# Performance work log

Hardware: AMD Instinct MI355X
Metric: run time of the kernel (lower is better)

The kernel has to match this reference:

```python
import jax, jax.numpy as jnp
import numpy as np

L, B, T, D, H, F, V = 4, 2, 1024, 1024, 16, 4096, 32000
DH = D // H
POWER = 4
EPS = 1e-6


def _anorm(x, gain):
    # y = g * x / (mean(|x|) + eps)  (L1 'diamond' norm)
    return gain * (x / (jnp.mean(jnp.abs(x), axis=-1, keepdims=True) + EPS))


def _rational_softmax(x):
    s = x / (jnp.abs(x) + 1.0)          # squash to (-1, 1)
    p = ((s + 1.0) * 0.5) ** POWER      # shift to (0,1), sharpen
    return p / (jnp.sum(p, axis=-1, keepdims=True) + EPS)


def setup_inputs() -> dict:
    key = jax.random.key(0)
    ks = jax.random.split(key, 12)
    w = 0.02  # weight scale for stability
    return {
        "idx": jax.random.randint(ks[0], (B, T), 0, V),
        "tok_emb": jax.random.normal(ks[1], (V, D), jnp.float32) * w,
        "pos_emb": jax.random.normal(ks[2], (T, D), jnp.float32) * w,
        "Wq": jax.random.normal(ks[3], (L, D, D), jnp.float32) * w,
        "bq": jnp.zeros((L, D), jnp.float32),
        "Wk": jax.random.normal(ks[4], (L, D, D), jnp.float32) * w,
        "bk": jnp.zeros((L, D), jnp.float32),
        "Wv": jax.random.normal(ks[5], (L, D, D), jnp.float32) * w,
        "bv": jnp.zeros((L, D), jnp.float32),
        "Wo": jax.random.normal(ks[6], (L, D, D), jnp.float32) * w,
        "bo": jnp.zeros((L, D), jnp.float32),
        "score_gain": jnp.full((L,), 4.0, jnp.float32),
        "norm1_gain": jnp.ones((L, D), jnp.float32),
        "norm2_gain": jnp.ones((L, D), jnp.float32),
        "W1": jax.random.normal(ks[7], (L, D, F), jnp.float32) * w,
        "b1": jnp.zeros((L, F), jnp.float32),
        "W2": jax.random.normal(ks[8], (L, F, D), jnp.float32) * w,
        "b2": jnp.zeros((L, D), jnp.float32),
        "final_gain": jnp.ones((D,), jnp.float32),
        "Wlm": jax.random.normal(ks[9], (D, V), jnp.float32) * w,
        "blm": jnp.zeros((V,), jnp.float32),
    }


def _forward(idx, tok_emb, pos_emb, Wq, bq, Wk, bk, Wv, bv, Wo, bo,
             score_gain, norm1_gain, norm2_gain, W1, b1, W2, b2,
             final_gain, Wlm, blm):
    Bx, Tx = idx.shape
    x = tok_emb[idx] + pos_emb[:Tx]                 # [B,T,D]
    mask = jnp.triu(jnp.ones((Tx, Tx), bool), 1)    # causal mask (True = masked)
    for l in range(L):
        # --- algebraic attention ---
        h = _anorm(x, norm1_gain[l])
        q = (h @ Wq[l] + bq[l]).reshape(Bx, Tx, H, DH).transpose(0, 2, 1, 3)
        k = (h @ Wk[l] + bk[l]).reshape(Bx, Tx, H, DH).transpose(0, 2, 1, 3)
        v = (h @ Wv[l] + bv[l]).reshape(Bx, Tx, H, DH).transpose(0, 2, 1, 3)
        scores = jnp.einsum('bhqd,bhkd->bhqk', q, k)
        scores = scores - jnp.mean(scores, axis=-1, keepdims=True)
        mad = jnp.mean(jnp.abs(scores), axis=-1, keepdims=True) + EPS
        scores = (scores / mad) * score_gain[l]
        scores = jnp.where(mask, -1000.0, scores)
        attn = _rational_softmax(scores)
        o = jnp.einsum('bhqk,bhkd->bhqd', attn, v)
        o = o.transpose(0, 2, 1, 3).reshape(Bx, Tx, D)
        x = x + (o @ Wo[l] + bo[l])
        # --- FFN with algebraic ReLU ---
        h = _anorm(x, norm2_gain[l])
        h = jnp.maximum(h @ W1[l] + b1[l], 0.0)
        x = x + (h @ W2[l] + b2[l])
    x = _anorm(x, final_gain)
    return x @ Wlm + blm                            # [B,T,V] logits


def reference(idx, tok_emb, pos_emb, Wq, bq, Wk, bk, Wv, bv, Wo, bo,
              score_gain, norm1_gain, norm2_gain, W1, b1, W2, b2,
              final_gain, Wlm, blm):
    return _forward(idx, tok_emb, pos_emb, Wq, bq, Wk, bk, Wv, bv, Wo, bo,
                    score_gain, norm1_gain, norm2_gain, W1, b1, W2, b2,
                    final_gain, Wlm, blm)
```

## Files before the change

kernel.cpp:

```cpp
#include <hip/hip_runtime.h>

typedef unsigned short u16;
typedef __bf16 bf16x8 __attribute__((ext_vector_type(8)));
typedef float f32x4 __attribute__((ext_vector_type(4)));
typedef unsigned int u32;

#define EPSF 1e-6f

__device__ __forceinline__ u16 f2bf(float f) {
  union { float f; unsigned u; } un; un.f = f;
  unsigned r = un.u + 0x7FFFu + ((un.u >> 16) & 1u);
  return (u16)(r >> 16);
}

__device__ __forceinline__ float block_sum(float v) {
  #pragma unroll
  for (int off = 32; off > 0; off >>= 1) v += __shfl_xor(v, off, 64);
  __shared__ float ws[4];
  const int w = threadIdx.x >> 6;
  __syncthreads();
  if ((threadIdx.x & 63) == 0) ws[w] = v;
  __syncthreads();
  return ws[0] + ws[1] + ws[2] + ws[3];
}

__device__ __forceinline__ void lds_cp16(const void* g, void* l) {
  __builtin_amdgcn_global_load_lds(
      (__attribute__((address_space(1))) void*)g,
      (__attribute__((address_space(3))) void*)l, 16, 0, 0);
}

__global__ __launch_bounds__(256) void embed_norm(
    const int* __restrict__ idx, const float* __restrict__ tok,
    const float* __restrict__ pos, const float* __restrict__ gain,
    float* __restrict__ x, u16* __restrict__ h) {
  const int row = blockIdx.x;
  const int tpos = row & 1023;
  const int token = idx[row];
  const int d = threadIdx.x * 4;
  const float4 a = *(const float4*)(tok + (long)token * 1024 + d);
  const float4 b = *(const float4*)(pos + (long)tpos * 1024 + d);
  float4 o; o.x = a.x + b.x; o.y = a.y + b.y; o.z = a.z + b.z; o.w = a.w + b.w;
  *(float4*)(x + (long)row * 1024 + d) = o;
  float s = fabsf(o.x) + fabsf(o.y) + fabsf(o.z) + fabsf(o.w);
  s = block_sum(s);
  const float scale = 1.0f / (s * (1.0f / 1024.0f) + EPSF);
  const float4 g = *(const float4*)(gain + d);
  ushort4 ov;
  ov.x = f2bf(o.x * g.x * scale);
  ov.y = f2bf(o.y * g.y * scale);
  ov.z = f2bf(o.z * g.z * scale);
  ov.w = f2bf(o.w * g.w * scale);
  *(ushort4*)(h + (long)row * 1024 + d) = ov;
}

__global__ __launch_bounds__(256) void anorm_kernel(
    const float* __restrict__ x, const float* __restrict__ gain,
    u16* __restrict__ h) {
  const int row = blockIdx.x;
  const int tid = threadIdx.x;
  const float4 v = *(const float4*)(x + (long)row * 1024 + tid * 4);
  float s = fabsf(v.x) + fabsf(v.y) + fabsf(v.z) + fabsf(v.w);
  s = block_sum(s);
  const float scale = 1.0f / (s * (1.0f / 1024.0f) + EPSF);
  const float4 g = *(const float4*)(gain + tid * 4);
  ushort4 o;
  o.x = f2bf(v.x * g.x * scale);
  o.y = f2bf(v.y * g.y * scale);
  o.z = f2bf(v.z * g.z * scale);
  o.w = f2bf(v.w * g.w * scale);
  *(ushort4*)(h + (long)row * 1024 + tid * 4) = o;
}

__global__ __launch_bounds__(512, 4) void attn_v4(
    const u16* __restrict__ qkv, const u16* __restrict__ v_t,
    u16* __restrict__ obuf, const float* __restrict__ score_gain, int l) {
  __shared__ float red1[2][4][16], red2[2][4][16], red3[2][4][16];
  __shared__ float Ured[2][4][16][68];
  __shared__ u16 Pl[8][640];
  const int qt = blockIdx.x, h = blockIdx.y, b = blockIdx.z;
  const int tid = threadIdx.x, w = tid >> 6, l64 = tid & 63;
  const int lq = l64 & 15, kgrp = l64 >> 4;
  const int wq = w >> 2, tq = w & 3;
  const int qglob = qt * 32 + wq * 16 + lq;
  const int qmax  = qt * 32 + wq * 16 + 15;
  const int tbase = tq * 256;
  const u16* Qg = qkv + (size_t)b * (1024 * 3072) + h * 64;
  const u16* Kg = Qg + 1024;
  const u16* Vt = v_t + (size_t)(b * 16 + h) * (64 * 1024);
  char* Pw = (char*)&Pl[w][0];

  bf16x8 qB0, qB1;
  {
    const u16* qp = Qg + (size_t)qglob * 3072 + (kgrp << 3);
    qB0 = *(const bf16x8*)qp;
    qB1 = *(const bf16x8*)(qp + 32);
  }

  f32x4 s[16];
  {
    const u16* Kl = Kg + (size_t)(tbase + lq) * 3072 + (kgrp << 3);
    #pragma unroll
    for (int tile = 0; tile < 16; tile++) {
      const u16* kp = Kl + (size_t)tile * (16 * 3072);
      const bf16x8 k0 = *(const bf16x8*)kp;
      const bf16x8 k1 = *(const bf16x8*)(kp + 32);
      f32x4 d = {0.f, 0.f, 0.f, 0.f};
      d = __builtin_amdgcn_mfma_f32_16x16x32_bf16(k0, qB0, d, 0, 0, 0);
      d = __builtin_amdgcn_mfma_f32_16x16x32_bf16(k1, qB1, d, 0, 0, 0);
      s[tile] = d;
    }
  }

  float ssum = 0.f;
  #pragma unroll
  for (int tile = 0; tile < 16; tile++)
    ssum += (s[tile][0] + s[tile][1]) + (s[tile][2] + s[tile][3]);
  ssum += __shfl_xor(ssum, 16, 64);
  ssum += __shfl_xor(ssum, 32, 64);
  if (l64 < 16) red1[wq][tq][l64] = ssum;
  __syncthreads();
  const float mean = (red1[wq][0][lq] + red1[wq][1][lq] +
                      red1[wq][2][lq] + red1[wq][3][lq]) * (1.0f / 1024.0f);

  float asum = 0.f;
  #pragma unroll
  for (int tile = 0; tile < 16; tile++)
    asum += fabsf(s[tile][0] - mean) + fabsf(s[tile][1] - mean) +
            fabsf(s[tile][2] - mean) + fabsf(s[tile][3] - mean);
  asum += __shfl_xor(asum, 16, 64);
  asum += __shfl_xor(asum, 32, 64);
  if (l64 < 16) red2[wq][tq][l64] = asum;
  __syncthreads();
  const float mad = (red2[wq][0][lq] + red2[wq][1][lq] +
                     red2[wq][2][lq] + red2[wq][3][lq]) * (1.0f / 1024.0f) + EPSF;
  const float gs = score_gain[l] / mad;

  float psum = 0.f;
  #pragma unroll
  for (int tile = 0; tile < 16; tile++) {
    #pragma unroll
    for (int j = 0; j < 4; j++) {
      const int t = tbase + tile * 16 + (kgrp << 2) + j;
      float sv = (s[tile][j] - mean) * gs;
      if (t > qglob) sv = -1000.0f;
      const float rr = sv / (fabsf(sv) + 1.0f);
      const float a1 = (rr + 1.0f) * 0.5f;
      const float a2 = a1 * a1;
      s[tile][j] = a2 * a2;
      psum += s[tile][j];
    }
  }

  f32x4 U[4] = {};
  #pragma unroll
  for (int c = 0; c < 8; c++) {
    const int t0 = tbase + c * 32;
    if (t0 <= qmax) {
      #pragma unroll
      for (int half = 0; half < 2; half++) {
        #pragma unroll
        for (int pr = 0; pr < 2; pr++) {
          const u32 pk = (u32)f2bf(s[2 * c + half][pr * 2]) |
                         ((u32)f2bf(s[2 * c + half][pr * 2 + 1]) << 16);
          *(u32*)(Pw + lq * 80 + half * 32 + (kgrp << 3) + (pr << 2)) = pk;
        }
      }
      asm volatile("s_waitcnt lgkmcnt(0)" ::: "memory");
      __builtin_amdgcn_sched_barrier(0);
      const bf16x8 pB = *(const bf16x8*)(Pw + lq * 80 + (kgrp << 4));
      #pragma unroll
      for (int dt = 0; dt < 4; dt++) {
        const bf16x8 vA = *(const bf16x8*)(Vt + (size_t)((dt << 4) + lq) * 1024 +
                                           t0 + (kgrp << 3));
        U[dt] = __builtin_amdgcn_mfma_f32_16x16x32_bf16(vA, pB, U[dt], 0, 0, 0);
      }
    }
  }

  psum += __shfl_xor(psum, 16, 64);
  psum += __shfl_xor(psum, 32, 64);
  if (l64 < 16) red3[wq][tq][l64] = psum;
  #pragma unroll
  for (int dt = 0; dt < 4; dt++)
    *(float4*)&Ured[wq][tq][lq][(dt << 4) + (kgrp << 2)] = *(const float4*)&U[dt];
  __syncthreads();

  {
    const int qq = tid >> 4, dhseg = (tid & 15) << 2;
    const int fwq = qq >> 4, flq = qq & 15;
    const float fps = red3[fwq][0][flq] + red3[fwq][1][flq] +
                      red3[fwq][2][flq] + red3[fwq][3][flq];
    const float oinv = 1.0f / (fps + EPSF);
    float4 u0 = *(const float4*)&Ured[fwq][0][flq][dhseg];
    const float4 u1 = *(const float4*)&Ured[fwq][1][flq][dhseg];
    const float4 u2 = *(const float4*)&Ured[fwq][2][flq][dhseg];
    const float4 u3 = *(const float4*)&Ured[fwq][3][flq][dhseg];
    u0.x = (u0.x + u1.x + u2.x + u3.x) * oinv;
    u0.y = (u0.y + u1.y + u2.y + u3.y) * oinv;
    u0.z = (u0.z + u1.z + u2.z + u3.z) * oinv;
    u0.w = (u0.w + u1.w + u2.w + u3.w) * oinv;
    ushort4 o;
    o.x = f2bf(u0.x); o.y = f2bf(u0.y); o.z = f2bf(u0.z); o.w = f2bf(u0.w);
    u16* dst = obuf + ((size_t)((b << 10) + qt * 32 + qq) << 10) + (h << 6) + dhseg;
    *(ushort4*)dst = o;
  }
}

__global__ void wconv_all(
    const float* __restrict__ Wq, const float* __restrict__ Wk,
    const float* __restrict__ Wv, const float* __restrict__ Wo,
    const float* __restrict__ W1, const float* __restrict__ W2,
    const float* __restrict__ Wlm,
    u16* __restrict__ wqkv_t, u16* __restrict__ wo_t,
    u16* __restrict__ w1_t, u16* __restrict__ w2_t, u16* __restrict__ wlm_t) {
  __shared__ float tile[64][65];
  const int bid = blockIdx.x;
  const float* src; u16* dst; int R, C, c0, r0;
  if (bid < 4096) {
    const int l = bid >> 10, m = (bid >> 8) & 3, t = bid & 255;
    if (m == 0)      src = Wq + (size_t)l * 1048576;
    else if (m == 1) src = Wk + (size_t)l * 1048576;
    else if (m == 2) src = Wv + (size_t)l * 1048576;
    else             src = Wo + (size_t)l * 1048576;
    dst = (m < 3) ? wqkv_t + ((size_t)l * 3072 + m * 1024) * 1024
                  : wo_t + (size_t)l * 1048576;
    R = 1024; C = 1024; c0 = (t & 15) << 6; r0 = (t >> 4) << 6;
  } else if (bid < 8192) {
    const int i = bid - 4096, l = i >> 10, t = i & 1023;
    src = W1 + (size_t)l * 4194304; dst = w1_t + (size_t)l * 4194304;
    R = 1024; C = 4096; c0 = (t & 63) << 6; r0 = (t >> 6) << 6;
  } else if (bid < 12288) {
    const int i = bid - 8192, l = i >> 10, t = i & 1023;
    src = W2 + (size_t)l * 4194304; dst = w2_t + (size_t)l * 4194304;
    R = 4096; C = 1024; c0 = (t & 15) << 6; r0 = (t >> 4) << 6;
  } else {
    const int i = bid - 12288;
    src = Wlm; dst = wlm_t;
    R = 1024; C = 32000; c0 = (i % 500) << 6; r0 = (i / 500) << 6;
  }
  const int tx = threadIdx.x, ty = threadIdx.y;
  #pragma unroll
  for (int i = 0; i < 16; i++)
    tile[i * 4 + ty][tx] = src[(long)(r0 + i * 4 + ty) * C + c0 + tx];
  __syncthreads();
  #pragma unroll
  for (int i = 0; i < 16; i++)
    dst[(long)(c0 + i * 4 + ty) * R + r0 + tx] = f2bf(tile[tx][i * 4 + ty]);
}

__global__ __launch_bounds__(256) void build_vt(
    const u16* __restrict__ qkv, u16* __restrict__ v_t) {
  __shared__ u16 tile[32][33];
  const int z = blockIdx.z, b = z >> 4, h = z & 15;
  const u16* src = qkv + (long)b * 1024 * 3072 + 2048 + h * 64;
  u16* dst = v_t + (long)z * 64 * 1024;
  const int t0 = blockIdx.x * 32, d0 = blockIdx.y * 32;
  const int tx = threadIdx.x, ty = threadIdx.y;
  #pragma unroll
  for (int i = 0; i < 4; i++)
    tile[ty + 8 * i][tx] = src[(long)(t0 + ty + 8 * i) * 3072 + d0 + tx];
  __syncthreads();
  #pragma unroll
  for (int i = 0; i < 4; i++)
    dst[(long)(d0 + ty + 8 * i) * 1024 + t0 + tx] = tile[tx][ty + 8 * i];
}

__global__ __launch_bounds__(256) void bias_concat(
    const float* __restrict__ bq, const float* __restrict__ bk,
    const float* __restrict__ bv, float* __restrict__ out) {
  const int i = blockIdx.x * 256 + threadIdx.x;
  const int l = i / 3072, j = i % 3072;
  float v;
  if (j < 1024)      v = bq[l * 1024 + j];
  else if (j < 2048) v = bk[l * 1024 + j - 1024];
  else               v = bv[l * 1024 + j - 2048];
  out[i] = v;
}

__global__ __launch_bounds__(256) void ffn2_reduce_norm(
    const float* __restrict__ part, const float* __restrict__ b2,
    float* __restrict__ x, const float* __restrict__ gain,
    u16* __restrict__ h) {
  const int row = blockIdx.x, c = threadIdx.x * 4;
  const float4 p0 = *(const float4*)(part + (size_t)row * 1024 + c);
  const float4 p1 = *(const float4*)(part + (size_t)(row + 2048) * 1024 + c);
  const float4 bb = *(const float4*)(b2 + c);
  float4 xv = *(float4*)(x + (size_t)row * 1024 + c);
  xv.x += p0.x + p1.x + bb.x;
  xv.y += p0.y + p1.y + bb.y;
  xv.z += p0.z + p1.z + bb.z;
  xv.w += p0.w + p1.w + bb.w;
  *(float4*)(x + (size_t)row * 1024 + c) = xv;
  float s = fabsf(xv.x) + fabsf(xv.y) + fabsf(xv.z) + fabsf(xv.w);
  s = block_sum(s);
  const float scale = 1.0f / (s * (1.0f / 1024.0f) + EPSF);
  const float4 g = *(const float4*)(gain + c);
  ushort4 o;
  o.x = f2bf(xv.x * g.x * scale);
  o.y = f2bf(xv.y * g.y * scale);
  o.z = f2bf(xv.z * g.z * scale);
  o.w = f2bf(xv.w * g.w * scale);
  *(ushort4*)(h + (size_t)row * 1024 + c) = o;
}

template <bool OUT_BF16, bool BIAS, bool RELU, bool RESID>
__global__ __launch_bounds__(512) void gemm256_kernel(
    const u16* __restrict__ A, long lda,
    const u16* __restrict__ Bt, long ldb,
    void* __restrict__ Cv, long ldc,
    const float* __restrict__ bias, const float* __restrict__ resid,
    int M, int N, int K, int nTM) {
  __shared__ u16 lds[65536];
  const int nwg = gridDim.x;
  const int qx = nwg >> 3, rx = nwg & 7;
  const int xcd = blockIdx.x & 7, seq = blockIdx.x >> 3;
  const int wg = (xcd < rx ? xcd * (qx + 1) : rx * (qx + 1) + (xcd - rx) * qx) + seq;
  const int tm = wg % nTM, tn = wg / nTM;
  const int rowA0 = tm * 256, rowB0 = tn * 256;

  const int t = threadIdx.x, w = t >> 6, l = t & 63;
  const int lrow = l & 15, kgrp = l >> 4;
  const int wr = w >> 2, wc = w & 3;

  const int srow = t >> 2;
  const int scol = ((t & 3) ^ ((t >> 3) & 3)) * 8;
  const u16* Asrc = A + (long)(rowA0 + srow) * lda + scol;
  const u16* Bsrc = Bt + (long)(rowB0 + srow) * ldb + scol;
  char* ldsB = (char*)lds;
  const int wbase = w * 1024;

  const int fswz = (kgrp ^ ((lrow >> 1) & 3)) * 8;
  const int aoff = (wr * 128 + lrow) * 32 + fswz;
  const int boff = 8192 + (wc * 64 + lrow) * 32 + fswz;

  f32x4 acc[8][4] = {};
  const int NT = K >> 5;

  #pragma unroll
  for (int pt = 0; pt < 3; pt++) {
    const int k0 = pt << 5;
    const int bb = pt * 32768;
    lds_cp16(Asrc + k0,                    ldsB + bb + wbase);
    lds_cp16(Asrc + (long)128 * lda + k0,  ldsB + bb + 8192 + wbase);
    lds_cp16(Bsrc + k0,                    ldsB + bb + 16384 + wbase);
    lds_cp16(Bsrc + (long)128 * ldb + k0,  ldsB + bb + 24576 + wbase);
  }

  for (int tt = 0; tt < NT; tt++) {
    const int rem = NT - 1 - tt;
    if (rem >= 2)      asm volatile("s_waitcnt vmcnt(8)" ::: "memory");
    else if (rem == 1) asm volatile("s_waitcnt vmcnt(4)" ::: "memory");
    else               asm volatile("s_waitcnt vmcnt(0)" ::: "memory");
    __builtin_amdgcn_sched_barrier(0);
    __builtin_amdgcn_s_barrier();

    const u16* buf = lds + (tt & 3) * 16384;
    const int stage = tt + 3 < NT;
    const int k0n = (tt + 3) << 5;
    const int bbn = ((tt + 3) & 3) * 32768;

    bf16x8 aF[4], bF[4], aS[4];
    #pragma unroll
    for (int m = 0; m < 4; m++) aF[m] = *(const bf16x8*)(buf + aoff + m * 512);
    #pragma unroll
    for (int n = 0; n < 4; n++) bF[n] = *(const bf16x8*)(buf + boff + n * 512);
    __builtin_amdgcn_sched_barrier(0);
    #pragma unroll
    for (int m = 0; m < 4; m++) aS[m] = *(const bf16x8*)(buf + aoff + (m + 4) * 512);
    if (stage) {
      lds_cp16(Asrc + k0n,                   ldsB + bbn + wbase);
      lds_cp16(Asrc + (long)128 * lda + k0n, ldsB + bbn + 8192 + wbase);
      lds_cp16(Bsrc + k0n,                   ldsB + bbn + 16384 + wbase);
      lds_cp16(Bsrc + (long)128 * ldb + k0n, ldsB + bbn + 24576 + wbase);
    }
    asm volatile("s_waitcnt lgkmcnt(4)" ::: "memory");
    __builtin_amdgcn_sched_barrier(0);
    __builtin_amdgcn_s_setprio(1);
    #pragma unroll
    for (int m = 0; m < 4; m++)
      #pragma unroll
      for (int n = 0; n < 4; n++)
        acc[m][n] = __builtin_amdgcn_mfma_f32_16x16x32_bf16(aF[m], bF[n], acc[m][n], 0, 0, 0);
    __builtin_amdgcn_s_setprio(0);
    asm volatile("s_waitcnt lgkmcnt(0)" ::: "memory");
    __builtin_amdgcn_sched_barrier(0);
    __builtin_amdgcn_s_setprio(1);
    #pragma unroll
    for (int m = 0; m < 4; m++)
      #pragma unroll
      for (int n = 0; n < 4; n++)
        acc[m + 4][n] = __builtin_amdgcn_mfma_f32_16x16x32_bf16(aS[m], bF[n], acc[m + 4][n], 0, 0, 0);
    __builtin_amdgcn_s_setprio(0);
  }

  float bvv[4];
  #pragma unroll
  for (int n = 0; n < 4; n++)
    bvv[n] = BIAS ? bias[rowB0 + wc * 64 + n * 16 + lrow] : 0.0f;
  #pragma unroll
  for (int m = 0; m < 8; m++) {
    const int row = rowA0 + wr * 128 + m * 16 + kgrp * 4;
    #pragma unroll
    for (int n = 0; n < 4; n++) {
      const int col = rowB0 + wc * 64 + n * 16 + lrow;
      #pragma unroll
      for (int j = 0; j < 4; j++) {
        float v = acc[m][n][j] + bvv[n];
        if (RELU) v = fmaxf(v, 0.0f);
        const long off = (long)(row + j) * ldc + col;
        if (RESID) v += resid[off];
        if (OUT_BF16) ((u16*)Cv)[off] = f2bf(v);
        else          ((float*)Cv)[off] = v;
      }
    }
  }
}

template <bool OUT_BF16, bool BIAS, bool RELU, bool RESID>
__global__ __launch_bounds__(256) void gemm128p(
    const u16* __restrict__ A, long lda, long sA,
    const u16* __restrict__ Bt, long ldb, long sB,
    void* __restrict__ Cv, long ldc, long sC,
    const float* __restrict__ bias, const float* __restrict__ resid,
    int M, int N, int K, int nTM) {
  __shared__ u16 lds[32768];
  const int nwg = gridDim.x;
  const int qx = nwg >> 3, rx = nwg & 7;
  const int xcd = blockIdx.x & 7, seq = blockIdx.x >> 3;
  const int wg = (xcd < rx ? xcd * (qx + 1) : rx * (qx + 1) + (xcd - rx) * qx) + seq;
  const int tm = wg % nTM, tn = wg / nTM;
  const int batch = blockIdx.y;
  A  += (long)batch * sA;
  Bt += (long)batch * sB;
  const int rowA0 = tm * 128, rowB0 = tn * 128;
  const int t = threadIdx.x, w = t >> 6, l = t & 63;
  const int lrow = l & 15, kgrp = l >> 4;
  const int wr = (w >> 1) << 6, wc = (w & 1) << 6;

  const int srow = t >> 2;
  const int scol = ((t & 3) ^ ((t >> 3) & 3)) * 8;
  const u16* Asrc = A + (long)(rowA0 + srow) * lda + scol;
  const u16* Bsrc = Bt + (long)(rowB0 + srow) * ldb + scol;
  char* ldsB = (char*)lds;
  const int wbase = w * 1024;

  const int swz8 = (kgrp ^ ((lrow >> 1) & 3)) * 8;
  const int aoff = (wr + lrow) * 32 + swz8;
  const int boff = 4096 + (wc + lrow) * 32 + swz8;

  f32x4 acc[4][4] = {};
  const int NT = K >> 5;

  #pragma unroll
  for (int pt = 0; pt < 3; pt++) {
    const int k0 = pt << 5;
    const int bb = pt * 16384;
    lds_cp16(Asrc + k0,                   ldsB + bb + wbase);
    lds_cp16(Asrc + (long)64 * lda + k0,  ldsB + bb + 4096 + wbase);
    lds_cp16(Bsrc + k0,                   ldsB + bb + 8192 + wbase);
    lds_cp16(Bsrc + (long)64 * ldb + k0,  ldsB + bb + 12288 + wbase);
  }

  for (int tt = 0; tt < NT; tt++) {
    const int rem = NT - 1 - tt;
    if (rem >= 2)      asm volatile("s_waitcnt vmcnt(8)" ::: "memory");
    else if (rem == 1) asm volatile("s_waitcnt vmcnt(4)" ::: "memory");
    else               asm volatile("s_waitcnt vmcnt(0)" ::: "memory");
    __builtin_amdgcn_sched_barrier(0);
    __builtin_amdgcn_s_barrier();

    const u16* buf = lds + (tt & 3) * 8192;
    const int stage = tt + 3 < NT;
    const int k0n = (tt + 3) << 5;
    const int bbn = ((tt + 3) & 3) * 16384;

    bf16x8 aF[4], bF[4];
    #pragma unroll
    for (int m = 0; m < 4; m++) aF[m] = *(const bf16x8*)(buf + aoff + m * 512);
    #pragma unroll
    for (int n = 0; n < 4; n++) bF[n] = *(const bf16x8*)(buf + boff + n * 512);
    if (stage) {
      lds_cp16(Asrc + k0n,                  ldsB + bbn + wbase);
      lds_cp16(Asrc + (long)64 * lda + k0n, ldsB + bbn + 4096 + wbase);
      lds_cp16(Bsrc + k0n,                  ldsB + bbn + 8192 + wbase);
      lds_cp16(Bsrc + (long)64 * ldb + k0n, ldsB + bbn + 12288 + wbase);
    }
    asm volatile("s_waitcnt lgkmcnt(0)" ::: "memory");
    __builtin_amdgcn_sched_barrier(0);
    __builtin_amdgcn_s_setprio(1);
    #pragma unroll
    for (int m = 0; m < 4; m++)
      #pragma unroll
      for (int n = 0; n < 4; n++)
        acc[m][n] = __builtin_amdgcn_mfma_f32_16x16x32_bf16(aF[m], bF[n], acc[m][n], 0, 0, 0);
    __builtin_amdgcn_s_setprio(0);
  }

  const long coff = (long)batch * sC;
  #pragma unroll
  for (int m = 0; m < 4; m++) {
    #pragma unroll
    for (int n = 0; n < 4; n++) {
      const int col = rowB0 + wc + n * 16 + lrow;
      #pragma unroll
      for (int j = 0; j < 4; j++) {
        const int row = rowA0 + wr + m * 16 + (kgrp << 2) + j;
        float v = acc[m][n][j];
        if (BIAS) v += bias[col];
        if (RELU) v = fmaxf(v, 0.0f);
        const long off = coff + (long)row * ldc + col;
        if (RESID) v += resid[off];
        if (OUT_BF16) ((u16*)Cv)[off] = f2bf(v);
        else          ((float*)Cv)[off] = v;
      }
    }
  }
}

extern "C" void kernel_launch(void* const* d_in, const int* in_sizes, int n_in,
                              void* d_out, int out_size, void* d_ws, size_t ws_size,
                              hipStream_t stream) {
  constexpr int Lc = 4, Tc = 1024, Dc = 1024, Hc = 16, Fc = 4096, DHc = 64;
  const int M = 2 * Tc;

  const int*   idxp       = (const int*)  d_in[0];
  const float* tok_emb    = (const float*)d_in[1];
  const float* pos_emb    = (const float*)d_in[2];
  const float* Wq         = (const float*)d_in[3];
  const float* bq         = (const float*)d_in[4];
  const float* Wk         = (const float*)d_in[5];
  const float* bk         = (const float*)d_in[6];
  const float* Wv         = (const float*)d_in[7];
  const float* bv         = (const float*)d_in[8];
  const float* Wo         = (const float*)d_in[9];
  const float* bo         = (const float*)d_in[10];
  const float* score_gain = (const float*)d_in[11];
  const float* norm1_gain = (const float*)d_in[12];
  const float* norm2_gain = (const float*)d_in[13];
  const float* W1         = (const float*)d_in[14];
  const float* b1         = (const float*)d_in[15];
  const float* W2         = (const float*)d_in[16];
  const float* b2         = (const float*)d_in[17];
  const float* final_gain = (const float*)d_in[18];
  const float* Wlm        = (const float*)d_in[19];
  const float* blm        = (const float*)d_in[20];

  char* p = (char*)d_ws;
  auto alloc = [&](size_t n) { char* r = p; p += (n + 255) & ~(size_t)255; return r; };
  u16*  wqkv_t = (u16*) alloc((size_t)Lc * 3072 * 1024 * 2);
  u16*  wo_t   = (u16*) alloc((size_t)Lc * 1024 * 1024 * 2);
  u16*  w1_t   = (u16*) alloc((size_t)Lc * 4096 * 1024 * 2);
  u16*  w2_t   = (u16*) alloc((size_t)Lc * 1024 * 4096 * 2);
  u16*  wlm_t  = (u16*) alloc((size_t)32000 * 1024 * 2);
  float* bqkv  = (float*)alloc((size_t)Lc * 3072 * 4);
  float* x     = (float*)alloc((size_t)M * 1024 * 4);
  u16*  hbuf   = (u16*) alloc((size_t)M * 1024 * 2);
  u16*  qkv    = (u16*) alloc((size_t)M * 3072 * 2);
  u16*  v_t    = (u16*) alloc((size_t)2 * Hc * DHc * Tc * 2);
  u16*  obuf   = (u16*) alloc((size_t)M * 1024 * 2);
  u16*  ffh    = (u16*) alloc((size_t)M * 4096 * 2);
  float* fpart = (float*)alloc((size_t)2 * M * 1024 * 4);

  wconv_all<<<20288, dim3(64, 4), 0, stream>>>(Wq, Wk, Wv, Wo, W1, W2, Wlm,
                                               wqkv_t, wo_t, w1_t, w2_t, wlm_t);
  bias_concat<<<48, 256, 0, stream>>>(bq, bk, bv, bqkv);
  embed_norm<<<M, 256, 0, stream>>>(idxp, tok_emb, pos_emb, norm1_gain, x, hbuf);

  for (int l = 0; l < Lc; l++) {
    gemm128p<true, true, false, false><<<dim3(16 * 24, 1), 256, 0, stream>>>(
        hbuf, 1024, 0, wqkv_t + (size_t)l * 3072 * 1024, 1024, 0,
        qkv, 3072, 0, bqkv + (size_t)l * 3072, nullptr, M, 3072, 1024, 16);
    build_vt<<<dim3(32, 2, 32), dim3(32, 8), 0, stream>>>(qkv, v_t);

    attn_v4<<<dim3(32, 16, 2), 512, 0, stream>>>(qkv, v_t, obuf, score_gain, l);

    gemm128p<false, true, false, true><<<dim3(16 * 8, 1), 256, 0, stream>>>(
        obuf, 1024, 0, wo_t + (size_t)l * 1024 * 1024, 1024, 0,
        x, 1024, 0, bo + (size_t)l * 1024, x, M, 1024, 1024, 16);
    anorm_kernel<<<M, 256, 0, stream>>>(x, norm2_gain + (size_t)l * Dc, hbuf);
    gemm256_kernel<true, true, true, false><<<dim3(128), 512, 0, stream>>>(
        hbuf, 1024, w1_t + (size_t)l * Fc * Dc, 1024,
        ffh, 4096, b1 + (size_t)l * Fc, nullptr, M, 4096, 1024, 8);
    gemm128p<false, false, false, false><<<dim3(128, 2), 256, 0, stream>>>(
        ffh, 4096, 2048, w2_t + (size_t)l * Dc * Fc, 4096, 2048,
        fpart, 1024, (long)M * 1024, nullptr, nullptr, M, 1024, 2048, 16);
    const float* gnext = (l < Lc - 1) ? (norm1_gain + (size_t)(l + 1) * Dc) : final_gain;
    ffn2_reduce_norm<<<M, 256, 0, stream>>>(fpart, b2 + (size_t)l * Dc, x, gnext, hbuf);
  }

  gemm256_kernel<false, true, false, false><<<dim3(1000), 512, 0, stream>>>(
      hbuf, 1024, wlm_t, 1024,
      d_out, 32000, blm, nullptr, M, 32000, 1024, 8);
}
```

Baseline: 1.013 ms.

## Fuse V transpose into QKV GEMM epilogue and use 128-tile GEMM everywhere

The QKV GEMM epilogue now writes the V columns straight into the transposed v_t layout through LDS, which removes the separate build_vt kernel. The 256x256 GEMM kernel is removed, and the FFN1 and LM-head GEMMs now run on the 128-tile kernel with more workgroups. The FFN2 split-K goes from 2 to 4 partitions, with a larger partial buffer and a wider reduction. Together these trade tile reuse for occupancy and better wave balance, at the cost of more partial-sum traffic.

```diff
diff --git a/kernel.cpp b/kernel.cpp
--- a/kernel.cpp
+++ b/kernel.cpp
@@ -249,23 +249,6 @@
     dst[(long)(c0 + i * 4 + ty) * R + r0 + tx] = f2bf(tile[tx][i * 4 + ty]);
 }
 
-__global__ __launch_bounds__(256) void build_vt(
-    const u16* __restrict__ qkv, u16* __restrict__ v_t) {
-  __shared__ u16 tile[32][33];
-  const int z = blockIdx.z, b = z >> 4, h = z & 15;
-  const u16* src = qkv + (long)b * 1024 * 3072 + 2048 + h * 64;
-  u16* dst = v_t + (long)z * 64 * 1024;
-  const int t0 = blockIdx.x * 32, d0 = blockIdx.y * 32;
-  const int tx = threadIdx.x, ty = threadIdx.y;
-  #pragma unroll
-  for (int i = 0; i < 4; i++)
-    tile[ty + 8 * i][tx] = src[(long)(t0 + ty + 8 * i) * 3072 + d0 + tx];
-  __syncthreads();
-  #pragma unroll
-  for (int i = 0; i < 4; i++)
-    dst[(long)(d0 + ty + 8 * i) * 1024 + t0 + tx] = tile[tx][ty + 8 * i];
-}
-
 __global__ __launch_bounds__(256) void bias_concat(
     const float* __restrict__ bq, const float* __restrict__ bk,
     const float* __restrict__ bv, float* __restrict__ out) {
@@ -285,12 +268,14 @@
   const int row = blockIdx.x, c = threadIdx.x * 4;
   const float4 p0 = *(const float4*)(part + (size_t)row * 1024 + c);
   const float4 p1 = *(const float4*)(part + (size_t)(row + 2048) * 1024 + c);
+  const float4 p2 = *(const float4*)(part + (size_t)(row + 4096) * 1024 + c);
+  const float4 p3 = *(const float4*)(part + (size_t)(row + 6144) * 1024 + c);
   const float4 bb = *(const float4*)(b2 + c);
   float4 xv = *(float4*)(x + (size_t)row * 1024 + c);
-  xv.x += p0.x + p1.x + bb.x;
-  xv.y += p0.y + p1.y + bb.y;
-  xv.z += p0.z + p1.z + bb.z;
-  xv.w += p0.w + p1.w + bb.w;
+  xv.x += (p0.x + p1.x) + (p2.x + p3.x) + bb.x;
+  xv.y += (p0.y + p1.y) + (p2.y + p3.y) + bb.y;
+  xv.z += (p0.z + p1.z) + (p2.z + p3.z) + bb.z;
+  xv.w += (p0.w + p1.w) + (p2.w + p3.w) + bb.w;
   *(float4*)(x + (size_t)row * 1024 + c) = xv;
   float s = fabsf(xv.x) + fabsf(xv.y) + fabsf(xv.z) + fabsf(xv.w);
   s = block_sum(s);
@@ -304,125 +289,13 @@
   *(ushort4*)(h + (size_t)row * 1024 + c) = o;
 }
 
-template <bool OUT_BF16, bool BIAS, bool RELU, bool RESID>
-__global__ __launch_bounds__(512) void gemm256_kernel(
-    const u16* __restrict__ A, long lda,
-    const u16* __restrict__ Bt, long ldb,
-    void* __restrict__ Cv, long ldc,
-    const float* __restrict__ bias, const float* __restrict__ resid,
-    int M, int N, int K, int nTM) {
-  __shared__ u16 lds[65536];
-  const int nwg = gridDim.x;
-  const int qx = nwg >> 3, rx = nwg & 7;
-  const int xcd = blockIdx.x & 7, seq = blockIdx.x >> 3;
-  const int wg = (xcd < rx ? xcd * (qx + 1) : rx * (qx + 1) + (xcd - rx) * qx) + seq;
-  const int tm = wg % nTM, tn = wg / nTM;
-  const int rowA0 = tm * 256, rowB0 = tn * 256;
-
-  const int t = threadIdx.x, w = t >> 6, l = t & 63;
-  const int lrow = l & 15, kgrp = l >> 4;
-  const int wr = w >> 2, wc = w & 3;
-
-  const int srow = t >> 2;
-  const int scol = ((t & 3) ^ ((t >> 3) & 3)) * 8;
-  const u16* Asrc = A + (long)(rowA0 + srow) * lda + scol;
-  const u16* Bsrc = Bt + (long)(rowB0 + srow) * ldb + scol;
-  char* ldsB = (char*)lds;
-  const int wbase = w * 1024;
-
-  const int fswz = (kgrp ^ ((lrow >> 1) & 3)) * 8;
-  const int aoff = (wr * 128 + lrow) * 32 + fswz;
-  const int boff = 8192 + (wc * 64 + lrow) * 32 + fswz;
-
-  f32x4 acc[8][4] = {};
-  const int NT = K >> 5;
-
-  #pragma unroll
-  for (int pt = 0; pt < 3; pt++) {
-    const int k0 = pt << 5;
-    const int bb = pt * 32768;
-    lds_cp16(Asrc + k0,                    ldsB + bb + wbase);
-    lds_cp16(Asrc + (long)128 * lda + k0,  ldsB + bb + 8192 + wbase);
-    lds_cp16(Bsrc + k0,                    ldsB + bb + 16384 + wbase);
-    lds_cp16(Bsrc + (long)128 * ldb + k0,  ldsB + bb + 24576 + wbase);
-  }
-
-  for (int tt = 0; tt < NT; tt++) {
-    const int rem = NT - 1 - tt;
-    if (rem >= 2)      asm volatile("s_waitcnt vmcnt(8)" ::: "memory");
-    else if (rem == 1) asm volatile("s_waitcnt vmcnt(4)" ::: "memory");
-    else               asm volatile("s_waitcnt vmcnt(0)" ::: "memory");
-    __builtin_amdgcn_sched_barrier(0);
-    __builtin_amdgcn_s_barrier();
-
-    const u16* buf = lds + (tt & 3) * 16384;
-    const int stage = tt + 3 < NT;
-    const int k0n = (tt + 3) << 5;
-    const int bbn = ((tt + 3) & 3) * 32768;
-
-    bf16x8 aF[4], bF[4], aS[4];
-    #pragma unroll
-    for (int m = 0; m < 4; m++) aF[m] = *(const bf16x8*)(buf + aoff + m * 512);
-    #pragma unroll
-    for (int n = 0; n < 4; n++) bF[n] = *(const bf16x8*)(buf + boff + n * 512);
-    __builtin_amdgcn_sched_barrier(0);
-    #pragma unroll
-    for (int m = 0; m < 4; m++) aS[m] = *(const bf16x8*)(buf + aoff + (m + 4) * 512);
-    if (stage) {
-      lds_cp16(Asrc + k0n,                   ldsB + bbn + wbase);
-      lds_cp16(Asrc + (long)128 * lda + k0n, ldsB + bbn + 8192 + wbase);
-      lds_cp16(Bsrc + k0n,                   ldsB + bbn + 16384 + wbase);
-      lds_cp16(Bsrc + (long)128 * ldb + k0n, ldsB + bbn + 24576 + wbase);
-    }
-    asm volatile("s_waitcnt lgkmcnt(4)" ::: "memory");
-    __builtin_amdgcn_sched_barrier(0);
-    __builtin_amdgcn_s_setprio(1);
-    #pragma unroll
-    for (int m = 0; m < 4; m++)
-      #pragma unroll
-      for (int n = 0; n < 4; n++)
-        acc[m][n] = __builtin_amdgcn_mfma_f32_16x16x32_bf16(aF[m], bF[n], acc[m][n], 0, 0, 0);
-    __builtin_amdgcn_s_setprio(0);
-    asm volatile("s_waitcnt lgkmcnt(0)" ::: "memory");
-    __builtin_amdgcn_sched_barrier(0);
-    __builtin_amdgcn_s_setprio(1);
-    #pragma unroll
-    for (int m = 0; m < 4; m++)
-      #pragma unroll
-      for (int n = 0; n < 4; n++)
-        acc[m + 4][n] = __builtin_amdgcn_mfma_f32_16x16x32_bf16(aS[m], bF[n], acc[m + 4][n], 0, 0, 0);
-    __builtin_amdgcn_s_setprio(0);
-  }
-
-  float bvv[4];
-  #pragma unroll
-  for (int n = 0; n < 4; n++)
-    bvv[n] = BIAS ? bias[rowB0 + wc * 64 + n * 16 + lrow] : 0.0f;
-  #pragma unroll
-  for (int m = 0; m < 8; m++) {
-    const int row = rowA0 + wr * 128 + m * 16 + kgrp * 4;
-    #pragma unroll
-    for (int n = 0; n < 4; n++) {
-      const int col = rowB0 + wc * 64 + n * 16 + lrow;
-      #pragma unroll
-      for (int j = 0; j < 4; j++) {
-        float v = acc[m][n][j] + bvv[n];
-        if (RELU) v = fmaxf(v, 0.0f);
-        const long off = (long)(row + j) * ldc + col;
-        if (RESID) v += resid[off];
-        if (OUT_BF16) ((u16*)Cv)[off] = f2bf(v);
-        else          ((float*)Cv)[off] = v;
-      }
-    }
-  }
-}
-
-template <bool OUT_BF16, bool BIAS, bool RELU, bool RESID>
+template <bool OUT_BF16, bool BIAS, bool RELU, bool RESID, bool VTOUT>
 __global__ __launch_bounds__(256) void gemm128p(
     const u16* __restrict__ A, long lda, long sA,
     const u16* __restrict__ Bt, long ldb, long sB,
     void* __restrict__ Cv, long ldc, long sC,
     const float* __restrict__ bias, const float* __restrict__ resid,
+    u16* __restrict__ vtout,
     int M, int N, int K, int nTM) {
   __shared__ u16 lds[32768];
   const int nwg = gridDim.x;
@@ -497,22 +370,54 @@
     __builtin_amdgcn_s_setprio(0);
   }
 
-  const long coff = (long)batch * sC;
-  #pragma unroll
-  for (int m = 0; m < 4; m++) {
-    #pragma unroll
-    for (int n = 0; n < 4; n++) {
-      const int col = rowB0 + wc + n * 16 + lrow;
-      #pragma unroll
-      for (int j = 0; j < 4; j++) {
-        const int row = rowA0 + wr + m * 16 + (kgrp << 2) + j;
-        float v = acc[m][n][j];
-        if (BIAS) v += bias[col];
-        if (RELU) v = fmaxf(v, 0.0f);
-        const long off = coff + (long)row * ldc + col;
-        if (RESID) v += resid[off];
-        if (OUT_BF16) ((u16*)Cv)[off] = f2bf(v);
-        else          ((float*)Cv)[off] = v;
+  if (VTOUT && rowB0 >= 2048) {
+    __syncthreads();
+    #pragma unroll
+    for (int m = 0; m < 4; m++) {
+      #pragma unroll
+      for (int n = 0; n < 4; n++) {
+        const int c = wc + n * 16 + lrow;
+        const int r = wr + m * 16 + (kgrp << 2);
+        ushort4 pk;
+        float v0 = acc[m][n][0], v1 = acc[m][n][1], v2 = acc[m][n][2], v3 = acc[m][n][3];
+        if (BIAS) {
+          const float bv = bias[rowB0 + c];
+          v0 += bv; v1 += bv; v2 += bv; v3 += bv;
+        }
+        pk.x = f2bf(v0); pk.y = f2bf(v1); pk.z = f2bf(v2); pk.w = f2bf(v3);
+        *(ushort4*)&lds[c * 136 + r] = pk;
+      }
+    }
+    __syncthreads();
+    {
+      const int c = t >> 1, half = t & 1;
+      const int dh = c & 63;
+      const int h = ((rowB0 - 2048) >> 6) + (c >> 6);
+      const int bb2 = rowA0 >> 10, t0 = rowA0 & 1023;
+      u16* dst = vtout + (((size_t)(bb2 * 16 + h)) << 16) + ((size_t)dh << 10) +
+                 t0 + half * 64;
+      #pragma unroll
+      for (int k = 0; k < 8; k++)
+        *(bf16x8*)(dst + k * 8) = *(const bf16x8*)&lds[c * 136 + half * 64 + k * 8];
+    }
+  } else {
+    const long coff = (long)batch * sC;
+    #pragma unroll
+    for (int m = 0; m < 4; m++) {
+      #pragma unroll
+      for (int n = 0; n < 4; n++) {
+        const int col = rowB0 + wc + n * 16 + lrow;
+        #pragma unroll
+        for (int j = 0; j < 4; j++) {
+          const int row = rowA0 + wr + m * 16 + (kgrp << 2) + j;
+          float v = acc[m][n][j];
+          if (BIAS) v += bias[col];
+          if (RELU) v = fmaxf(v, 0.0f);
+          const long off = coff + (long)row * ldc + col;
+          if (RESID) v += resid[off];
+          if (OUT_BF16) ((u16*)Cv)[off] = f2bf(v);
+          else          ((float*)Cv)[off] = v;
+        }
       }
     }
   }
@@ -560,7 +465,7 @@
   u16*  v_t    = (u16*) alloc((size_t)2 * Hc * DHc * Tc * 2);
   u16*  obuf   = (u16*) alloc((size_t)M * 1024 * 2);
   u16*  ffh    = (u16*) alloc((size_t)M * 4096 * 2);
-  float* fpart = (float*)alloc((size_t)2 * M * 1024 * 4);
+  float* fpart = (float*)alloc((size_t)4 * M * 1024 * 4);
 
   wconv_all<<<20288, dim3(64, 4), 0, stream>>>(Wq, Wk, Wv, Wo, W1, W2, Wlm,
                                                wqkv_t, wo_t, w1_t, w2_t, wlm_t);
@@ -568,28 +473,27 @@
   embed_norm<<<M, 256, 0, stream>>>(idxp, tok_emb, pos_emb, norm1_gain, x, hbuf);
 
   for (int l = 0; l < Lc; l++) {
-    gemm128p<true, true, false, false><<<dim3(16 * 24, 1), 256, 0, stream>>>(
+    gemm128p<true, true, false, false, true><<<dim3(16 * 24, 1), 256, 0, stream>>>(
         hbuf, 1024, 0, wqkv_t + (size_t)l * 3072 * 1024, 1024, 0,
-        qkv, 3072, 0, bqkv + (size_t)l * 3072, nullptr, M, 3072, 1024, 16);
-    build_vt<<<dim3(32, 2, 32), dim3(32, 8), 0, stream>>>(qkv, v_t);
+        qkv, 3072, 0, bqkv + (size_t)l * 3072, nullptr, v_t, M, 3072, 1024, 16);
 
     attn_v4<<<dim3(32, 16, 2), 512, 0, stream>>>(qkv, v_t, obuf, score_gain, l);
 
-    gemm128p<false, true, false, true><<<dim3(16 * 8, 1), 256, 0, stream>>>(
+    gemm128p<false, true, false, true, false><<<dim3(16 * 8, 1), 256, 0, stream>>>(
         obuf, 1024, 0, wo_t + (size_t)l * 1024 * 1024, 1024, 0,
-        x, 1024, 0, bo + (size_t)l * 1024, x, M, 1024, 1024, 16);
+        x, 1024, 0, bo + (size_t)l * 1024, x, nullptr, M, 1024, 1024, 16);
     anorm_kernel<<<M, 256, 0, stream>>>(x, norm2_gain + (size_t)l * Dc, hbuf);
-    gemm256_kernel<true, true, true, false><<<dim3(128), 512, 0, stream>>>(
-        hbuf, 1024, w1_t + (size_t)l * Fc * Dc, 1024,
-        ffh, 4096, b1 + (size_t)l * Fc, nullptr, M, 4096, 1024, 8);
-    gemm128p<false, false, false, false><<<dim3(128, 2), 256, 0, stream>>>(
-        ffh, 4096, 2048, w2_t + (size_t)l * Dc * Fc, 4096, 2048,
-        fpart, 1024, (long)M * 1024, nullptr, nullptr, M, 1024, 2048, 16);
+    gemm128p<true, true, true, false, false><<<dim3(16 * 32, 1), 256, 0, stream>>>(
+        hbuf, 1024, 0, w1_t + (size_t)l * Fc * Dc, 1024, 0,
+        ffh, 4096, 0, b1 + (size_t)l * Fc, nullptr, nullptr, M, 4096, 1024, 16);
+    gemm128p<false, false, false, false, false><<<dim3(128, 4), 256, 0, stream>>>(
+        ffh, 4096, 1024, w2_t + (size_t)l * Dc * Fc, 4096, 1024,
+        fpart, 1024, (long)M * 1024, nullptr, nullptr, nullptr, M, 1024, 1024, 16);
     const float* gnext = (l < Lc - 1) ? (norm1_gain + (size_t)(l + 1) * Dc) : final_gain;
     ffn2_reduce_norm<<<M, 256, 0, stream>>>(fpart, b2 + (size_t)l * Dc, x, gnext, hbuf);
   }
 
-  gemm256_kernel<false, true, false, false><<<dim3(1000), 512, 0, stream>>>(
-      hbuf, 1024, wlm_t, 1024,
-      d_out, 32000, blm, nullptr, M, 32000, 1024, 8);
-}
+  gemm128p<false, true, false, false, false><<<dim3(16 * 250, 1), 256, 0, stream>>>(
+      hbuf, 1024, 0, wlm_t, 1024, 0,
+      d_out, 32000, 0, blm, nullptr, nullptr, M, 32000, 1024, 16);
+}
```

Measured after the change: 1.022 ms. Within noise of the previous version (+0.8%).

## Fuse V-transpose into QKV GEMM, retile FFN GEMMs, vectorize weight conversion

Applied to the files above, without the earlier changes.

The QKV GEMM epilogue now writes V tiles transposed through LDS straight into v_t, so the separate build_vt kernel is dropped. FFN1 moves from the 256-tile kernel to the 128-tile kernel with more workgroups. FFN2 uses a 4-way split-K whose partials are reduced in the norm kernel, which doubles the partial-sum buffer traffic. The weight conversion uses float4 loads and ushort4 stores, and the 256 GEMM main loop staggers its A/B LDS loads to cut register pressure, at the cost of a full lgkmcnt wait.

```diff
diff --git a/kernel.cpp b/kernel.cpp
--- a/kernel.cpp
+++ b/kernel.cpp
@@ -240,30 +240,24 @@
     R = 1024; C = 32000; c0 = (i % 500) << 6; r0 = (i / 500) << 6;
   }
   const int tx = threadIdx.x, ty = threadIdx.y;
-  #pragma unroll
-  for (int i = 0; i < 16; i++)
-    tile[i * 4 + ty][tx] = src[(long)(r0 + i * 4 + ty) * C + c0 + tx];
+  const int cg = (tx & 15) << 2;
+  const int rg = tx >> 4;
+  #pragma unroll
+  for (int i = 0; i < 4; i++) {
+    const int row = i * 16 + ty * 4 + rg;
+    const float4 v = *(const float4*)&src[(long)(r0 + row) * C + c0 + cg];
+    tile[row][cg] = v.x; tile[row][cg + 1] = v.y;
+    tile[row][cg + 2] = v.z; tile[row][cg + 3] = v.w;
+  }
   __syncthreads();
   #pragma unroll
-  for (int i = 0; i < 16; i++)
-    dst[(long)(c0 + i * 4 + ty) * R + r0 + tx] = f2bf(tile[tx][i * 4 + ty]);
-}
-
-__global__ __launch_bounds__(256) void build_vt(
-    const u16* __restrict__ qkv, u16* __restrict__ v_t) {
-  __shared__ u16 tile[32][33];
-  const int z = blockIdx.z, b = z >> 4, h = z & 15;
-  const u16* src = qkv + (long)b * 1024 * 3072 + 2048 + h * 64;
-  u16* dst = v_t + (long)z * 64 * 1024;
-  const int t0 = blockIdx.x * 32, d0 = blockIdx.y * 32;
-  const int tx = threadIdx.x, ty = threadIdx.y;
-  #pragma unroll
-  for (int i = 0; i < 4; i++)
-    tile[ty + 8 * i][tx] = src[(long)(t0 + ty + 8 * i) * 3072 + d0 + tx];
-  __syncthreads();
-  #pragma unroll
-  for (int i = 0; i < 4; i++)
-    dst[(long)(d0 + ty + 8 * i) * 1024 + t0 + tx] = tile[tx][ty + 8 * i];
+  for (int i = 0; i < 4; i++) {
+    const int c = i * 16 + ty * 4 + rg;
+    ushort4 o;
+    o.x = f2bf(tile[cg][c]);     o.y = f2bf(tile[cg + 1][c]);
+    o.z = f2bf(tile[cg + 2][c]); o.w = f2bf(tile[cg + 3][c]);
+    *(ushort4*)&dst[(long)(c0 + c) * R + r0 + cg] = o;
+  }
 }
 
 __global__ __launch_bounds__(256) void bias_concat(
@@ -285,12 +279,14 @@
   const int row = blockIdx.x, c = threadIdx.x * 4;
   const float4 p0 = *(const float4*)(part + (size_t)row * 1024 + c);
   const float4 p1 = *(const float4*)(part + (size_t)(row + 2048) * 1024 + c);
+  const float4 p2 = *(const float4*)(part + (size_t)(row + 4096) * 1024 + c);
+  const float4 p3 = *(const float4*)(part + (size_t)(row + 6144) * 1024 + c);
   const float4 bb = *(const float4*)(b2 + c);
   float4 xv = *(float4*)(x + (size_t)row * 1024 + c);
-  xv.x += p0.x + p1.x + bb.x;
-  xv.y += p0.y + p1.y + bb.y;
-  xv.z += p0.z + p1.z + bb.z;
-  xv.w += p0.w + p1.w + bb.w;
+  xv.x += (p0.x + p1.x) + (p2.x + p3.x) + bb.x;
+  xv.y += (p0.y + p1.y) + (p2.y + p3.y) + bb.y;
+  xv.z += (p0.z + p1.z) + (p2.z + p3.z) + bb.z;
+  xv.w += (p0.w + p1.w) + (p2.w + p3.w) + bb.w;
   *(float4*)(x + (size_t)row * 1024 + c) = xv;
   float s = fabsf(xv.x) + fabsf(xv.y) + fabsf(xv.z) + fabsf(xv.w);
   s = block_sum(s);
@@ -360,21 +356,16 @@
     const int k0n = (tt + 3) << 5;
     const int bbn = ((tt + 3) & 3) * 32768;
 
-    bf16x8 aF[4], bF[4], aS[4];
+    bf16x8 aF[4], bF[4];
     #pragma unroll
     for (int m = 0; m < 4; m++) aF[m] = *(const bf16x8*)(buf + aoff + m * 512);
     #pragma unroll
     for (int n = 0; n < 4; n++) bF[n] = *(const bf16x8*)(buf + boff + n * 512);
-    __builtin_amdgcn_sched_barrier(0);
-    #pragma unroll
-    for (int m = 0; m < 4; m++) aS[m] = *(const bf16x8*)(buf + aoff + (m + 4) * 512);
     if (stage) {
       lds_cp16(Asrc + k0n,                   ldsB + bbn + wbase);
       lds_cp16(Asrc + (long)128 * lda + k0n, ldsB + bbn + 8192 + wbase);
-      lds_cp16(Bsrc + k0n,                   ldsB + bbn + 16384 + wbase);
-      lds_cp16(Bsrc + (long)128 * ldb + k0n, ldsB + bbn + 24576 + wbase);
-    }
-    asm volatile("s_waitcnt lgkmcnt(4)" ::: "memory");
+    }
+    asm volatile("s_waitcnt lgkmcnt(0)" ::: "memory");
     __builtin_amdgcn_sched_barrier(0);
     __builtin_amdgcn_s_setprio(1);
     #pragma unroll
@@ -383,6 +374,13 @@
       for (int n = 0; n < 4; n++)
         acc[m][n] = __builtin_amdgcn_mfma_f32_16x16x32_bf16(aF[m], bF[n], acc[m][n], 0, 0, 0);
     __builtin_amdgcn_s_setprio(0);
+
+    #pragma unroll
+    for (int m = 0; m < 4; m++) aF[m] = *(const bf16x8*)(buf + aoff + (m + 4) * 512);
+    if (stage) {
+      lds_cp16(Bsrc + k0n,                   ldsB + bbn + 16384 + wbase);
+      lds_cp16(Bsrc + (long)128 * ldb + k0n, ldsB + bbn + 24576 + wbase);
+    }
     asm volatile("s_waitcnt lgkmcnt(0)" ::: "memory");
     __builtin_amdgcn_sched_barrier(0);
     __builtin_amdgcn_s_setprio(1);
@@ -390,7 +388,7 @@
     for (int m = 0; m < 4; m++)
       #pragma unroll
       for (int n = 0; n < 4; n++)
-        acc[m + 4][n] = __builtin_amdgcn_mfma_f32_16x16x32_bf16(aS[m], bF[n], acc[m + 4][n], 0, 0, 0);
+        acc[m + 4][n] = __builtin_amdgcn_mfma_f32_16x16x32_bf16(aF[m], bF[n], acc[m + 4][n], 0, 0, 0);
     __builtin_amdgcn_s_setprio(0);
   }
 
@@ -417,12 +415,13 @@
   }
 }
 
-template <bool OUT_BF16, bool BIAS, bool RELU, bool RESID>
+template <bool OUT_BF16, bool BIAS, bool RELU, bool RESID, bool VTOUT>
 __global__ __launch_bounds__(256) void gemm128p(
     const u16* __restrict__ A, long lda, long sA,
     const u16* __restrict__ Bt, long ldb, long sB,
     void* __restrict__ Cv, long ldc, long sC,
     const float* __restrict__ bias, const float* __restrict__ resid,
+    u16* __restrict__ vtout,
     int M, int N, int K, int nTM) {
   __shared__ u16 lds[32768];
   const int nwg = gridDim.x;
@@ -497,22 +496,54 @@
     __builtin_amdgcn_s_setprio(0);
   }
 
-  const long coff = (long)batch * sC;
-  #pragma unroll
-  for (int m = 0; m < 4; m++) {
-    #pragma unroll
-    for (int n = 0; n < 4; n++) {
-      const int col = rowB0 + wc + n * 16 + lrow;
-      #pragma unroll
-      for (int j = 0; j < 4; j++) {
-        const int row = rowA0 + wr + m * 16 + (kgrp << 2) + j;
-        float v = acc[m][n][j];
-        if (BIAS) v += bias[col];
-        if (RELU) v = fmaxf(v, 0.0f);
-        const long off = coff + (long)row * ldc + col;
-        if (RESID) v += resid[off];
-        if (OUT_BF16) ((u16*)Cv)[off] = f2bf(v);
-        else          ((float*)Cv)[off] = v;
+  if (VTOUT && rowB0 >= 2048) {
+    __syncthreads();
+    #pragma unroll
+    for (int m = 0; m < 4; m++) {
+      #pragma unroll
+      for (int n = 0; n < 4; n++) {
+        const int c = wc + n * 16 + lrow;
+        const int r = wr + m * 16 + (kgrp << 2);
+        ushort4 pk;
+        float v0 = acc[m][n][0], v1 = acc[m][n][1], v2 = acc[m][n][2], v3 = acc[m][n][3];
+        if (BIAS) {
+          const float bv = bias[rowB0 + c];
+          v0 += bv; v1 += bv; v2 += bv; v3 += bv;
+        }
+        pk.x = f2bf(v0); pk.y = f2bf(v1); pk.z = f2bf(v2); pk.w = f2bf(v3);
+        *(ushort4*)&lds[c * 136 + r] = pk;
+      }
+    }
+    __syncthreads();
+    {
+      const int c = t >> 1, half = t & 1;
+      const int dh = c & 63;
+      const int h = ((rowB0 - 2048) >> 6) + (c >> 6);
+      const int bb2 = rowA0 >> 10, t0 = rowA0 & 1023;
+      u16* dst = vtout + (((size_t)(bb2 * 16 + h)) << 16) + ((size_t)dh << 10) +
+                 t0 + half * 64;
+      #pragma unroll
+      for (int k = 0; k < 8; k++)
+        *(bf16x8*)(dst + k * 8) = *(const bf16x8*)&lds[c * 136 + half * 64 + k * 8];
+    }
+  } else {
+    const long coff = (long)batch * sC;
+    #pragma unroll
+    for (int m = 0; m < 4; m++) {
+      #pragma unroll
+      for (int n = 0; n < 4; n++) {
+        const int col = rowB0 + wc + n * 16 + lrow;
+        #pragma unroll
+        for (int j = 0; j < 4; j++) {
+          const int row = rowA0 + wr + m * 16 + (kgrp << 2) + j;
+          float v = acc[m][n][j];
+          if (BIAS) v += bias[col];
+          if (RELU) v = fmaxf(v, 0.0f);
+          const long off = coff + (long)row * ldc + col;
+          if (RESID) v += resid[off];
+          if (OUT_BF16) ((u16*)Cv)[off] = f2bf(v);
+          else          ((float*)Cv)[off] = v;
+        }
       }
     }
   }
@@ -560,7 +591,7 @@
   u16*  v_t    = (u16*) alloc((size_t)2 * Hc * DHc * Tc * 2);
   u16*  obuf   = (u16*) alloc((size_t)M * 1024 * 2);
   u16*  ffh    = (u16*) alloc((size_t)M * 4096 * 2);
-  float* fpart = (float*)alloc((size_t)2 * M * 1024 * 4);
+  float* fpart = (float*)alloc((size_t)4 * M * 1024 * 4);
 
   wconv_all<<<20288, dim3(64, 4), 0, stream>>>(Wq, Wk, Wv, Wo, W1, W2, Wlm,
                                                wqkv_t, wo_t, w1_t, w2_t, wlm_t);
@@ -568,23 +599,22 @@
   embed_norm<<<M, 256, 0, stream>>>(idxp, tok_emb, pos_emb, norm1_gain, x, hbuf);
 
   for (int l = 0; l < Lc; l++) {
-    gemm128p<true, true, false, false><<<dim3(16 * 24, 1), 256, 0, stream>>>(
+    gemm128p<true, true, false, false, true><<<dim3(16 * 24, 1), 256, 0, stream>>>(
         hbuf, 1024, 0, wqkv_t + (size_t)l * 3072 * 1024, 1024, 0,
-        qkv, 3072, 0, bqkv + (size_t)l * 3072, nullptr, M, 3072, 1024, 16);
-    build_vt<<<dim3(32, 2, 32), dim3(32, 8), 0, stream>>>(qkv, v_t);
+        qkv, 3072, 0, bqkv + (size_t)l * 3072, nullptr, v_t, M, 3072, 1024, 16);
 
     attn_v4<<<dim3(32, 16, 2), 512, 0, stream>>>(qkv, v_t, obuf, score_gain, l);
 
-    gemm128p<false, true, false, true><<<dim3(16 * 8, 1), 256, 0, stream>>>(
+    gemm128p<false, true, false, true, false><<<dim3(16 * 8, 1), 256, 0, stream>>>(
         obuf, 1024, 0, wo_t + (size_t)l * 1024 * 1024, 1024, 0,
-        x, 1024, 0, bo + (size_t)l * 1024, x, M, 1024, 1024, 16);
+        x, 1024, 0, bo + (size_t)l * 1024, x, nullptr, M, 1024, 1024, 16);
     anorm_kernel<<<M, 256, 0, stream>>>(x, norm2_gain + (size_t)l * Dc, hbuf);
-    gemm256_kernel<true, true, true, false><<<dim3(128), 512, 0, stream>>>(
-        hbuf, 1024, w1_t + (size_t)l * Fc * Dc, 1024,
-        ffh, 4096, b1 + (size_t)l * Fc, nullptr, M, 4096, 1024, 8);
-    gemm128p<false, false, false, false><<<dim3(128, 2), 256, 0, stream>>>(
-        ffh, 4096, 2048, w2_t + (size_t)l * Dc * Fc, 4096, 2048,
-        fpart, 1024, (long)M * 1024, nullptr, nullptr, M, 1024, 2048, 16);
+    gemm128p<true, true, true, false, false><<<dim3(16 * 32, 1), 256, 0, stream>>>(
+        hbuf, 1024, 0, w1_t + (size_t)l * Fc * Dc, 1024, 0,
+        ffh, 4096, 0, b1 + (size_t)l * Fc, nullptr, nullptr, M, 4096, 1024, 16);
+    gemm128p<false, false, false, false, false><<<dim3(128, 4), 256, 0, stream>>>(
+        ffh, 4096, 1024, w2_t + (size_t)l * Dc * Fc, 4096, 1024,
+        fpart, 1024, (long)M * 1024, nullptr, nullptr, nullptr, M, 1024, 1024, 16);
     const float* gnext = (l < Lc - 1) ? (norm1_gain + (size_t)(l + 1) * Dc) : final_gain;
     ffn2_reduce_norm<<<M, 256, 0, stream>>>(fpart, b2 + (size_t)l * Dc, x, gnext, hbuf);
   }
```

Result: faster. 990.9 us (-2.2%).
